# Performance work log

Measured on AMD Instinct MI355X. Metric: run time of the kernel, lower is better.

## Reference

```python
import jax, jax.numpy as jnp
import numpy as np

NUM_CLASSES = 3
BBOX_W, OBJ_W, CLS_W = 0.05, 1.0, 0.5


def setup_inputs() -> dict:
    key = jax.random.key(0)
    kp, kc, kcl, kv = jax.random.split(key, 4)
    B, C, H, W, N = 64, 8, 256, 256, 200
    pred = jax.random.normal(kp, (B, C, H, W), dtype=jnp.float32)
    # normalized (x, y, w, h) in (0, 1) so every label is in-bounds with positive coord sum
    coords = jax.random.uniform(kc, (B, N, 4), jnp.float32, 1e-3, 0.999)
    cls_id = jax.random.randint(kcl, (B, N), 0, NUM_CLASSES).astype(jnp.float32)
    invalid = jax.random.uniform(kv, (B, N)) < 0.25
    cls_id = jnp.where(invalid, -1.0, cls_id)
    targets = jnp.concatenate([cls_id[..., None], coords], axis=-1)  # [B, N, 5]
    return {"pred": pred, "targets": targets}


def _bce_with_logits(logits, z):
    # stable: softplus(x) - x*z  ==  max(x,0) - x*z + log(1+exp(-|x|))
    return jax.nn.softplus(logits) - logits * z


def reference(pred, targets):
    B, C, H, W = pred.shape
    cls_id = targets[..., 0]            # [B, N]
    coords = targets[..., 1:5]          # [B, N, 4] = (x, y, w, h)

    valid = (cls_id >= 0) & (coords.sum(-1) > 0)
    # int() truncation of x*w / y*h (coords nonnegative -> floor)
    xpix = (coords[..., 0] * W).astype(jnp.int32)
    ypix = (coords[..., 1] * H).astype(jnp.int32)
    in_bounds = (xpix >= 0) & (xpix < W) & (ypix >= 0) & (ypix < H)
    mask = (valid & in_bounds).astype(pred.dtype)   # [B, N]

    xs = jnp.clip(xpix, 0, W - 1)
    ys = jnp.clip(ypix, 0, H - 1)
    bidx = jnp.arange(B)[:, None]
    # gather pred[b, :, y, x] for every label -> [B, N, C]
    p = pred[bidx, :, ys, xs]

    # bbox: MSE mean over the 4 coords (torch detaches target_coords via torch.tensor())
    tgt = jax.lax.stop_gradient(coords)
    bbox = jnp.mean((p[..., :4] - tgt) ** 2, axis=-1)            # [B, N]
    # objectness: BCEWithLogits against 1.0 (mean over 1 element)
    obj = _bce_with_logits(p[..., 4], 1.0)                       # [B, N]
    # class: BCEWithLogits against one-hot(class_id), mean over classes
    onehot = jax.nn.one_hot(jnp.clip(cls_id, 0, None).astype(jnp.int32),
                            NUM_CLASSES, dtype=pred.dtype)       # [B, N, K]
    cls_l = jnp.mean(_bce_with_logits(p[..., 5:5 + NUM_CLASSES], onehot), axis=-1)

    bbox_sum = jnp.sum(bbox * mask)
    obj_sum = jnp.sum(obj * mask)
    cls_sum = jnp.sum(cls_l * mask)
    total = BBOX_W * bbox_sum + OBJ_W * obj_sum + CLS_W * cls_sum
    # (total, bbox, obj, cls) matching the dict values of the torch module
    return jnp.stack([total, bbox_sum, obj_sum, cls_sum])
```

## Files before the change

kernel.cpp:

```cpp
#include <hip/hip_runtime.h>
#include <math.h>

#define BD 64
#define ND 200
#define CD 8
#define HD 256
#define WD 256
#define HW (HD * WD)
#define NBOX (BD * ND)
#define NTHR (NBOX * CD)
#define NBLK (NTHR / 256)

__device__ __forceinline__ float softplus_f(float x) {
    return fmaxf(x, 0.0f) + log1pf(expf(-fabsf(x)));
}

__global__ __launch_bounds__(256) void yolo_partial(const float* __restrict__ pred,
                                                    const float* __restrict__ targets,
                                                    float* __restrict__ partial) {
    const int tid = blockIdx.x * 256 + threadIdx.x;
    const int box = tid >> 3;
    const int c   = tid & 7;
    const int b   = box / ND;

    const float* t = targets + (size_t)box * 5;
    const float cls_id = t[0];
    const float c0 = t[1], c1 = t[2], c2 = t[3], c3 = t[4];

    const bool valid = (cls_id >= 0.0f) && ((c0 + c1 + c2 + c3) > 0.0f);
    const int xpix = (int)(c0 * (float)WD);
    const int ypix = (int)(c1 * (float)HD);
    const bool inb = (xpix >= 0) && (xpix < WD) && (ypix >= 0) && (ypix < HD);
    const bool m = valid && inb;

    float bbox = 0.0f, obj = 0.0f, clsl = 0.0f;
    if (m) {
        const int xs = min(max(xpix, 0), WD - 1);
        const int ys = min(max(ypix, 0), HD - 1);
        const float p = pred[(size_t)b * CD * HW + (size_t)c * HW + (size_t)ys * WD + xs];

        if (c < 4) {
            const float tc = (c == 0) ? c0 : (c == 1) ? c1 : (c == 2) ? c2 : c3;
            const float d = p - tc;
            bbox = 0.25f * d * d;
        } else if (c == 4) {
            obj = softplus_f(p) - p;
        } else {
            const int ci = (int)fmaxf(cls_id, 0.0f);
            const float z = ((c - 5) == ci) ? 1.0f : 0.0f;
            clsl = (softplus_f(p) - p * z) * (1.0f / 3.0f);
        }
    }

#pragma unroll
    for (int off = 32; off > 0; off >>= 1) {
        bbox += __shfl_down(bbox, off, 64);
        obj  += __shfl_down(obj,  off, 64);
        clsl += __shfl_down(clsl, off, 64);
    }

    __shared__ float sb[4], so[4], sc[4];
    const int wave = threadIdx.x >> 6;
    const int lane = threadIdx.x & 63;
    if (lane == 0) { sb[wave] = bbox; so[wave] = obj; sc[wave] = clsl; }
    __syncthreads();

    if (threadIdx.x == 0) {
        partial[blockIdx.x * 3 + 0] = sb[0] + sb[1] + sb[2] + sb[3];
        partial[blockIdx.x * 3 + 1] = so[0] + so[1] + so[2] + so[3];
        partial[blockIdx.x * 3 + 2] = sc[0] + sc[1] + sc[2] + sc[3];
    }
}

__global__ __launch_bounds__(256) void yolo_final(const float* __restrict__ partial,
                                                  float* __restrict__ out) {
    const int t = threadIdx.x;
    float tb = 0.0f, to = 0.0f, tc = 0.0f;
    for (int i = t; i < NBLK; i += 256) {
        tb += partial[i * 3 + 0];
        to += partial[i * 3 + 1];
        tc += partial[i * 3 + 2];
    }
#pragma unroll
    for (int off = 32; off > 0; off >>= 1) {
        tb += __shfl_down(tb, off, 64);
        to += __shfl_down(to, off, 64);
        tc += __shfl_down(tc, off, 64);
    }
    __shared__ float sb[4], so[4], sc[4];
    const int wave = t >> 6;
    const int lane = t & 63;
    if (lane == 0) { sb[wave] = tb; so[wave] = to; sc[wave] = tc; }
    __syncthreads();

    if (t == 0) {
        const float B = sb[0] + sb[1] + sb[2] + sb[3];
        const float O = so[0] + so[1] + so[2] + so[3];
        const float C = sc[0] + sc[1] + sc[2] + sc[3];
        out[0] = 0.05f * B + 1.0f * O + 0.5f * C;
        out[1] = B;
        out[2] = O;
        out[3] = C;
    }
}

extern "C" void kernel_launch(void* const* d_in, const int* in_sizes, int n_in,
                              void* d_out, int out_size, void* d_ws, size_t ws_size,
                              hipStream_t stream) {
    const float* pred    = (const float*)d_in[0];
    const float* targets = (const float*)d_in[1];
    float* out     = (float*)d_out;
    float* partial = (float*)d_ws;

    yolo_partial<<<NBLK, 256, 0, stream>>>(pred, targets, partial);
    yolo_final<<<1, 256, 0, stream>>>(partial, out);
}
```

Before: 166.6 us.

## Assign one box per thread, gathering all eight channels per thread

Remaps the partial kernel from one thread per (box, channel) to one thread per box. Each thread loads all eight channel values and computes the bbox, objectness and class terms itself. Blocks become single 64-thread waves, so the shared-memory cross-wave reduction and its barrier go away, and partials are stored in a struct-of-arrays layout. This cuts the redundant target reads and thread count, but each thread now issues eight scattered loads and there are fewer threads to hide latency.

```diff
diff --git a/kernel.cpp b/kernel.cpp
--- a/kernel.cpp
+++ b/kernel.cpp
@@ -8,19 +8,16 @@
 #define WD 256
 #define HW (HD * WD)
 #define NBOX (BD * ND)
-#define NTHR (NBOX * CD)
-#define NBLK (NTHR / 256)
+#define PBLK (NBOX / 64)
 
 __device__ __forceinline__ float softplus_f(float x) {
     return fmaxf(x, 0.0f) + log1pf(expf(-fabsf(x)));
 }
 
-__global__ __launch_bounds__(256) void yolo_partial(const float* __restrict__ pred,
-                                                    const float* __restrict__ targets,
-                                                    float* __restrict__ partial) {
-    const int tid = blockIdx.x * 256 + threadIdx.x;
-    const int box = tid >> 3;
-    const int c   = tid & 7;
+__global__ __launch_bounds__(64) void yolo_partial(const float* __restrict__ pred,
+                                                   const float* __restrict__ targets,
+                                                   float* __restrict__ partial) {
+    const int box = blockIdx.x * 64 + threadIdx.x;
     const int b   = box / ND;
 
     const float* t = targets + (size_t)box * 5;
@@ -31,25 +28,24 @@
     const int xpix = (int)(c0 * (float)WD);
     const int ypix = (int)(c1 * (float)HD);
     const bool inb = (xpix >= 0) && (xpix < WD) && (ypix >= 0) && (ypix < HD);
-    const bool m = valid && inb;
 
     float bbox = 0.0f, obj = 0.0f, clsl = 0.0f;
-    if (m) {
+    if (valid && inb) {
         const int xs = min(max(xpix, 0), WD - 1);
         const int ys = min(max(ypix, 0), HD - 1);
-        const float p = pred[(size_t)b * CD * HW + (size_t)c * HW + (size_t)ys * WD + xs];
+        const float* p = pred + (size_t)b * CD * HW + (size_t)ys * WD + xs;
 
-        if (c < 4) {
-            const float tc = (c == 0) ? c0 : (c == 1) ? c1 : (c == 2) ? c2 : c3;
-            const float d = p - tc;
-            bbox = 0.25f * d * d;
-        } else if (c == 4) {
-            obj = softplus_f(p) - p;
-        } else {
-            const int ci = (int)fmaxf(cls_id, 0.0f);
-            const float z = ((c - 5) == ci) ? 1.0f : 0.0f;
-            clsl = (softplus_f(p) - p * z) * (1.0f / 3.0f);
-        }
+        const float p0 = p[0 * HW], p1 = p[1 * HW], p2 = p[2 * HW], p3 = p[3 * HW];
+        const float p4 = p[4 * HW], p5 = p[5 * HW], p6 = p[6 * HW], p7 = p[7 * HW];
+
+        const float d0 = p0 - c0, d1 = p1 - c1, d2 = p2 - c2, d3 = p3 - c3;
+        bbox = 0.25f * (d0 * d0 + d1 * d1 + d2 * d2 + d3 * d3);
+
+        obj = softplus_f(p4) - p4;
+
+        const int ci = (int)cls_id;
+        const float psel = (ci == 0) ? p5 : (ci == 1) ? p6 : p7;
+        clsl = (softplus_f(p5) + softplus_f(p6) + softplus_f(p7) - psel) * (1.0f / 3.0f);
     }
 
 #pragma unroll
@@ -59,27 +55,22 @@
         clsl += __shfl_down(clsl, off, 64);
     }
 
-    __shared__ float sb[4], so[4], sc[4];
-    const int wave = threadIdx.x >> 6;
-    const int lane = threadIdx.x & 63;
-    if (lane == 0) { sb[wave] = bbox; so[wave] = obj; sc[wave] = clsl; }
-    __syncthreads();
-
     if (threadIdx.x == 0) {
-        partial[blockIdx.x * 3 + 0] = sb[0] + sb[1] + sb[2] + sb[3];
-        partial[blockIdx.x * 3 + 1] = so[0] + so[1] + so[2] + so[3];
-        partial[blockIdx.x * 3 + 2] = sc[0] + sc[1] + sc[2] + sc[3];
+        partial[blockIdx.x]            = bbox;
+        partial[PBLK + blockIdx.x]     = obj;
+        partial[2 * PBLK + blockIdx.x] = clsl;
     }
 }
 
-__global__ __launch_bounds__(256) void yolo_final(const float* __restrict__ partial,
-                                                  float* __restrict__ out) {
+__global__ __launch_bounds__(64) void yolo_final(const float* __restrict__ partial,
+                                                 float* __restrict__ out) {
     const int t = threadIdx.x;
     float tb = 0.0f, to = 0.0f, tc = 0.0f;
-    for (int i = t; i < NBLK; i += 256) {
-        tb += partial[i * 3 + 0];
-        to += partial[i * 3 + 1];
-        tc += partial[i * 3 + 2];
+#pragma unroll
+    for (int i = t; i < PBLK; i += 64) {
+        tb += partial[i];
+        to += partial[PBLK + i];
+        tc += partial[2 * PBLK + i];
     }
 #pragma unroll
     for (int off = 32; off > 0; off >>= 1) {
@@ -87,20 +78,11 @@
         to += __shfl_down(to, off, 64);
         tc += __shfl_down(tc, off, 64);
     }
-    __shared__ float sb[4], so[4], sc[4];
-    const int wave = t >> 6;
-    const int lane = t & 63;
-    if (lane == 0) { sb[wave] = tb; so[wave] = to; sc[wave] = tc; }
-    __syncthreads();
-
     if (t == 0) {
-        const float B = sb[0] + sb[1] + sb[2] + sb[3];
-        const float O = so[0] + so[1] + so[2] + so[3];
-        const float C = sc[0] + sc[1] + sc[2] + sc[3];
-        out[0] = 0.05f * B + 1.0f * O + 0.5f * C;
-        out[1] = B;
-        out[2] = O;
-        out[3] = C;
+        out[0] = 0.05f * tb + 1.0f * to + 0.5f * tc;
+        out[1] = tb;
+        out[2] = to;
+        out[3] = tc;
     }
 }
 
@@ -112,6 +94,6 @@
     float* out     = (float*)d_out;
     float* partial = (float*)d_ws;
 
-    yolo_partial<<<NBLK, 256, 0, stream>>>(pred, targets, partial);
-    yolo_final<<<1, 256, 0, stream>>>(partial, out);
+    yolo_partial<<<PBLK, 64, 0, stream>>>(pred, targets, partial);
+    yolo_final<<<1, 64, 0, stream>>>(partial, out);
 }
```

Result: no change. 165.2 us (-0.9%).
